# Optimization experiments

Hardware: AMD Instinct MI355X
Metric: run time of the kernel (lower is better)

The kernel has to match this reference:

```python
import jax, jax.numpy as jnp
import numpy as np

M, N, DIM, B = 32000, 2048, 1024, 2048  # vocab, hidden, embed dim, batch
SIGMA = 20.0


def setup_inputs() -> dict:
    key = jax.random.key(0)
    ks = jax.random.split(key, 16)
    u = lambda k, shape: jax.random.uniform(k, shape, dtype=jnp.float32)
    return {
        "input_text": jax.random.randint(ks[0], (B,), 0, M),
        "h_prev": jax.random.normal(ks[1], (N, B), dtype=jnp.float32),
        "C_prev": jax.random.normal(ks[2], (N, B), dtype=jnp.float32),
        "emb": jax.random.normal(ks[3], (M, DIM), dtype=jnp.float32),
        "W_A": u(ks[4], (M, N)) / SIGMA,
        "W_C": u(ks[5], (N, N + DIM)) / SIGMA,
        "W_f": u(ks[6], (N, N + DIM)) / SIGMA,
        "W_o": u(ks[7], (N, N + DIM)) / SIGMA,
        "W_i": u(ks[8], (N, N + DIM)) / SIGMA,
        "b_A": u(ks[9], (M, 1)),
        "b_C": u(ks[10], (N, 1)),
        "b_f": u(ks[11], (N, 1)),
        "b_o": u(ks[12], (N, 1)),
        "b_i": u(ks[13], (N, 1)),
    }


def reference(input_text, h_prev, C_prev, emb, W_A, W_C, W_f, W_o, W_i,
              b_A, b_C, b_f, b_o, b_i):
    x = emb[input_text].T                     # [dim, B]
    z = jnp.concatenate([h_prev, x], axis=0)  # [n+dim, B]
    f = jax.nn.sigmoid(W_f @ z + b_f)
    i = jax.nn.sigmoid(W_i @ z + b_i)
    o = jax.nn.sigmoid(W_o @ z + b_o)
    tildeC = jnp.tanh(W_C @ z + b_C)
    C = f * C_prev + i * tildeC
    h = o * jnp.tanh(C)
    y = W_A @ h + b_A                         # [m, B]
    return (y, h, C)
```

## Files before the change

### kernel.cpp

```cpp
#include <hip/hip_runtime.h>

#define DM 32000
#define DN 2048
#define DD 1024
#define DB 2048
#define DKG 3072

typedef __attribute__((ext_vector_type(4))) float floatx4;
typedef __attribute__((ext_vector_type(8))) short shortx8;

__device__ inline unsigned int f2bf(float f) {
    unsigned int u = __builtin_bit_cast(unsigned int, f);
    u += 0x7fffu + ((u >> 16) & 1u);
    return u >> 16;
}

__device__ inline unsigned int cvt_pk_bf16(float lo, float hi) {
    unsigned int r;
    asm("v_cvt_pk_bf16_f32 %0, %1, %2" : "=v"(r) : "v"(lo), "v"(hi));
    return r;
}

__device__ inline void gld_lds16(const void* g, void* l) {
    __builtin_amdgcn_global_load_lds(
        (const __attribute__((address_space(1))) unsigned int*)g,
        (__attribute__((address_space(3))) unsigned int*)l,
        16, 0, 0);
}

__device__ inline float fast_sigmoid(float x) { return 1.0f / (1.0f + __expf(-x)); }
__device__ inline float fast_tanh(float x) { return 1.0f - 2.0f / (__expf(2.0f * x) + 1.0f); }

__global__ __launch_bounds__(256) void transpose_h_kernel(
    const float* __restrict__ h_prev, unsigned short* __restrict__ z_t)
{
    __shared__ unsigned short T[64 * 66];
    int t = threadIdx.x;
    int b0 = blockIdx.x * 64, k0 = blockIdx.y * 64;
    int bi = t & 63, wv = t >> 6;
    #pragma unroll
    for (int i = 0; i < 16; i++) {
        int kl = wv + i * 4;
        float v = h_prev[(size_t)(k0 + kl) * DB + b0 + bi];
        T[kl * 66 + bi] = (unsigned short)f2bf(v);
    }
    __syncthreads();
    #pragma unroll
    for (int i = 0; i < 16; i++) {
        int r = wv + i * 4;
        z_t[(size_t)(b0 + r) * DKG + k0 + bi] = T[bi * 66 + r];
    }
}

__global__ __launch_bounds__(256) void emb_gather_kernel(
    const int* __restrict__ idx, const float* __restrict__ emb,
    unsigned short* __restrict__ z_t)
{
    int b = blockIdx.x;
    int row = idx[b];
    int t = threadIdx.x;
    const floatx4 v = *(const floatx4*)(&emb[(size_t)row * DD + t * 4]);
    unsigned int p0 = (f2bf(v[1]) << 16) | f2bf(v[0]);
    unsigned int p1 = (f2bf(v[3]) << 16) | f2bf(v[2]);
    *(uint2*)(&z_t[(size_t)b * DKG + DN + t * 4]) = make_uint2(p0, p1);
}

__global__ __launch_bounds__(256) void wconv_kernel(
    const float* __restrict__ src, unsigned short* __restrict__ dst)
{
    size_t i = ((size_t)blockIdx.x * 256 + threadIdx.x) * 8;
    floatx4 v0 = *(const floatx4*)(src + i);
    floatx4 v1 = *(const floatx4*)(src + i + 4);
    uint4 p;
    p.x = cvt_pk_bf16(v0[0], v0[1]);
    p.y = cvt_pk_bf16(v0[2], v0[3]);
    p.z = cvt_pk_bf16(v1[0], v1[1]);
    p.w = cvt_pk_bf16(v1[2], v1[3]);
    *(uint4*)(dst + i) = p;
}


__global__ __launch_bounds__(256, 3) void gemm_wa_kernel(
    const unsigned short* __restrict__ A, const unsigned short* __restrict__ Bt,
    float* __restrict__ C, const float* __restrict__ bias)
{
    __shared__ unsigned short As[128 * 64];
    __shared__ unsigned short Bs[128 * 64];
    const int K = DN;
    int t = threadIdx.x;
    int lane = t & 63, wave = t >> 6;
    int wm = (wave >> 1) * 64, wn = (wave & 1) * 64;
    size_t m0 = (size_t)blockIdx.y * 128, n0 = (size_t)blockIdx.x * 128;
    int mrow = lane & 15, kgrp = lane >> 4, l7 = lane & 7;
    int r8 = t >> 3, lsl = t & 7;
    int ss = lsl ^ (r8 & 7);

    floatx4 acc[4][4] = {};

    for (int k0 = 0; k0 < K; k0 += 64) {
        #pragma unroll
        for (int i = 0; i < 4; i++) {
            int row = i * 32 + r8;
            gld_lds16(A  + (m0 + row) * (size_t)K + k0 + ss * 8,
                      &As[(i * 256 + wave * 64) * 8]);
            gld_lds16(Bt + (n0 + row) * (size_t)K + k0 + ss * 8,
                      &Bs[(i * 256 + wave * 64) * 8]);
        }
        __syncthreads();
        #pragma unroll
        for (int ks = 0; ks < 2; ks++) {
            int so = ((ks * 4 + kgrp) ^ l7) * 8;
            shortx8 af[4], bfv[4];
            #pragma unroll
            for (int mi = 0; mi < 4; mi++)
                af[mi] = *(const shortx8*)(&As[(wm + mi * 16 + mrow) * 64 + so]);
            #pragma unroll
            for (int ni = 0; ni < 4; ni++)
                bfv[ni] = *(const shortx8*)(&Bs[(wn + ni * 16 + mrow) * 64 + so]);
            #pragma unroll
            for (int mi = 0; mi < 4; mi++)
                #pragma unroll
                for (int ni = 0; ni < 4; ni++)
                    acc[mi][ni] = __builtin_amdgcn_mfma_f32_16x16x32_bf16(
                        af[mi], bfv[ni], acc[mi][ni], 0, 0, 0);
        }
        __syncthreads();
    }

    int cn = lane & 15, rb = kgrp * 4;
    #pragma unroll
    for (int mi = 0; mi < 4; mi++) {
        #pragma unroll
        for (int r = 0; r < 4; r++) {
            size_t row = m0 + wm + mi * 16 + rb + r;
            float bv = bias[row];
            #pragma unroll
            for (int ni = 0; ni < 4; ni++)
                C[row * DB + n0 + wn + ni * 16 + cn] = acc[mi][ni][r] + bv;
        }
    }
}

__global__ __launch_bounds__(256, 3) void gemm_gates_kernel(
    const float* __restrict__ A0, const float* __restrict__ A1,
    const float* __restrict__ A2, const float* __restrict__ A3,
    const unsigned short* __restrict__ Bt,
    float* __restrict__ C0, float* __restrict__ C1,
    float* __restrict__ C2, float* __restrict__ C3)
{
    __shared__ unsigned short As[128 * 64];
    __shared__ unsigned short Bs[128 * 64];
    const int K = DKG;
    int t = threadIdx.x;
    int lane = t & 63, wave = t >> 6;
    int wm = (wave >> 1) * 64, wn = (wave & 1) * 64;
    int zz = blockIdx.z;
    const float* A = (zz == 0) ? A0 : (zz == 1) ? A1 : (zz == 2) ? A2 : A3;
    float* Cout    = (zz == 0) ? C0 : (zz == 1) ? C1 : (zz == 2) ? C2 : C3;
    size_t m0 = (size_t)blockIdx.y * 128, n0 = (size_t)blockIdx.x * 128;
    int mrow = lane & 15, kgrp = lane >> 4, l7 = lane & 7;
    int r8 = t >> 3, lsl = t & 7;
    int ss = lsl ^ (r8 & 7);

    floatx4 acc[4][4] = {};

    for (int k0 = 0; k0 < K; k0 += 64) {
        #pragma unroll
        for (int i = 0; i < 4; i++) {
            int row = i * 32 + r8;
            gld_lds16(Bt + (n0 + row) * (size_t)K + k0 + ss * 8,
                      &Bs[(i * 256 + wave * 64) * 8]);
        }
        #pragma unroll
        for (int i = 0; i < 4; i++) {
            int row = i * 32 + r8;
            const float* src = A + (m0 + row) * (size_t)K + k0 + lsl * 8;
            floatx4 v0 = *(const floatx4*)(src);
            floatx4 v1 = *(const floatx4*)(src + 4);
            uint4 p;
            p.x = cvt_pk_bf16(v0[0], v0[1]);
            p.y = cvt_pk_bf16(v0[2], v0[3]);
            p.z = cvt_pk_bf16(v1[0], v1[1]);
            p.w = cvt_pk_bf16(v1[2], v1[3]);
            *(uint4*)(&As[(row * 8 + ss) * 8]) = p;
        }
        __syncthreads();
        #pragma unroll
        for (int ks = 0; ks < 2; ks++) {
            int so = ((ks * 4 + kgrp) ^ l7) * 8;
            shortx8 af[4], bfv[4];
            #pragma unroll
            for (int mi = 0; mi < 4; mi++)
                af[mi] = *(const shortx8*)(&As[(wm + mi * 16 + mrow) * 64 + so]);
            #pragma unroll
            for (int ni = 0; ni < 4; ni++)
                bfv[ni] = *(const shortx8*)(&Bs[(wn + ni * 16 + mrow) * 64 + so]);
            #pragma unroll
            for (int mi = 0; mi < 4; mi++)
                #pragma unroll
                for (int ni = 0; ni < 4; ni++)
                    acc[mi][ni] = __builtin_amdgcn_mfma_f32_16x16x32_bf16(
                        af[mi], bfv[ni], acc[mi][ni], 0, 0, 0);
        }
        __syncthreads();
    }

    int cn = lane & 15, rb = kgrp * 4;
    #pragma unroll
    for (int mi = 0; mi < 4; mi++) {
        #pragma unroll
        for (int r = 0; r < 4; r++) {
            size_t row = m0 + wm + mi * 16 + rb + r;
            #pragma unroll
            for (int ni = 0; ni < 4; ni++)
                Cout[row * DB + n0 + wn + ni * 16 + cn] = acc[mi][ni][r];
        }
    }
}

__global__ __launch_bounds__(256) void pointwise_kernel(
    const float* __restrict__ Pf, const float* __restrict__ Pi,
    const float* __restrict__ Po, const float* __restrict__ Pc,
    const float* __restrict__ C_prev,
    const float* __restrict__ b_f, const float* __restrict__ b_i,
    const float* __restrict__ b_o, const float* __restrict__ b_C,
    float* __restrict__ outH, float* __restrict__ outC,
    unsigned short* __restrict__ h_t)
{
    __shared__ unsigned short T[64 * 66];
    int t = threadIdx.x;
    int b0 = blockIdx.x * 64, n0 = blockIdx.y * 64;
    int bi = t & 63, wv = t >> 6;
    #pragma unroll
    for (int i = 0; i < 16; i++) {
        int nl = wv + i * 4;
        size_t idx = (size_t)(n0 + nl) * DB + b0 + bi;
        float f  = fast_sigmoid(Pf[idx] + b_f[n0 + nl]);
        float ii = fast_sigmoid(Pi[idx] + b_i[n0 + nl]);
        float o  = fast_sigmoid(Po[idx] + b_o[n0 + nl]);
        float tc = fast_tanh(Pc[idx] + b_C[n0 + nl]);
        float C  = f * C_prev[idx] + ii * tc;
        float h  = o * fast_tanh(C);
        outC[idx] = C;
        outH[idx] = h;
        T[nl * 66 + bi] = (unsigned short)f2bf(h);
    }
    __syncthreads();
    #pragma unroll
    for (int i = 0; i < 16; i++) {
        int r = wv + i * 4;
        h_t[(size_t)(b0 + r) * DN + n0 + bi] = T[bi * 66 + r];
    }
}

extern "C" void kernel_launch(void* const* d_in, const int* in_sizes, int n_in,
                              void* d_out, int out_size, void* d_ws, size_t ws_size,
                              hipStream_t stream)
{
    const int*   input_text = (const int*)d_in[0];
    const float* h_prev = (const float*)d_in[1];
    const float* C_prev = (const float*)d_in[2];
    const float* emb    = (const float*)d_in[3];
    const float* W_A    = (const float*)d_in[4];
    const float* W_C    = (const float*)d_in[5];
    const float* W_f    = (const float*)d_in[6];
    const float* W_o    = (const float*)d_in[7];
    const float* W_i    = (const float*)d_in[8];
    const float* b_A    = (const float*)d_in[9];
    const float* b_C    = (const float*)d_in[10];
    const float* b_f    = (const float*)d_in[11];
    const float* b_o    = (const float*)d_in[12];
    const float* b_i    = (const float*)d_in[13];

    char* ws = (char*)d_ws;
    unsigned short* z_t = (unsigned short*)ws;
    float* Pf = (float*)(ws + 12582912);
    float* Pi = (float*)(ws + 12582912 + 1 * 16777216);
    float* Po = (float*)(ws + 12582912 + 2 * 16777216);
    float* Pc = (float*)(ws + 12582912 + 3 * 16777216);
    unsigned short* h_t = (unsigned short*)(ws + 12582912 + 4 * 16777216);
    unsigned short* wa  = (unsigned short*)ws;

    float* y    = (float*)d_out;
    float* outH = y + (size_t)DM * DB;
    float* outC = outH + (size_t)DN * DB;

    transpose_h_kernel<<<dim3(32, 32), 256, 0, stream>>>(h_prev, z_t);
    emb_gather_kernel<<<dim3(2048), 256, 0, stream>>>(input_text, emb, z_t);

    gemm_gates_kernel<<<dim3(16, 16, 4), 256, 0, stream>>>(
        W_f, W_i, W_o, W_C, z_t, Pf, Pi, Po, Pc);

    pointwise_kernel<<<dim3(32, 32), 256, 0, stream>>>(
        Pf, Pi, Po, Pc, C_prev, b_f, b_i, b_o, b_C, outH, outC, h_t);

    wconv_kernel<<<dim3(16000), 256, 0, stream>>>(W_A, wa);
    gemm_wa_kernel<<<dim3(16, 125), 256, 0, stream>>>(wa, h_t, y, b_A);
    wconv_kernel<<<dim3(16000), 256, 0, stream>>>(W_A + (size_t)16000 * DN, wa);
    gemm_wa_kernel<<<dim3(16, 125), 256, 0, stream>>>(
        wa, h_t, y + (size_t)16000 * DB, b_A + 16000);
}
```

Before: 1.023 ms.

## Pre-convert gate weights to bf16 and unify GEMMs with XCD-aware tile swizzle

The four gate weight matrices are converted to bf16 up front, into the output y buffer used as scratch, and stacked. The gate GEMM then becomes one launch of a shared bf16 GEMM kernel that loads A asynchronously straight into LDS, instead of converting fp32 A in registers inside the K loop. The shared kernel also remaps block IDs so that blocks scheduled on the same XCD work on contiguous tiles, aiming for better L2 reuse, and it handles an optional bias. The cost is extra conversion passes over about 100 MB of fp32 weights plus the writes of their bf16 copies.

Measured after the change: 979.3 us. 1.04x faster.

```diff
diff --git a/kernel.cpp b/kernel.cpp
--- a/kernel.cpp
+++ b/kernel.cpp
@@ -79,18 +79,21 @@
     *(uint4*)(dst + i) = p;
 }
 
-
-__global__ __launch_bounds__(256, 3) void gemm_wa_kernel(
+__global__ __launch_bounds__(256, 3) void gemm_bt16_kernel(
     const unsigned short* __restrict__ A, const unsigned short* __restrict__ Bt,
-    float* __restrict__ C, const float* __restrict__ bias)
+    float* __restrict__ C, const float* __restrict__ bias, int K)
 {
     __shared__ unsigned short As[128 * 64];
     __shared__ unsigned short Bs[128 * 64];
-    const int K = DN;
     int t = threadIdx.x;
     int lane = t & 63, wave = t >> 6;
     int wm = (wave >> 1) * 64, wn = (wave & 1) * 64;
-    size_t m0 = (size_t)blockIdx.y * 128, n0 = (size_t)blockIdx.x * 128;
+
+    int nwg = gridDim.x * gridDim.y;
+    int flat = blockIdx.y * gridDim.x + blockIdx.x;
+    int swz = (flat & 7) * (nwg >> 3) + (flat >> 3);
+    size_t m0 = (size_t)(swz >> 4) * 128, n0 = (size_t)(swz & 15) * 128;
+
     int mrow = lane & 15, kgrp = lane >> 4, l7 = lane & 7;
     int r8 = t >> 3, lsl = t & 7;
     int ss = lsl ^ (r8 & 7);
@@ -133,87 +136,10 @@
         #pragma unroll
         for (int r = 0; r < 4; r++) {
             size_t row = m0 + wm + mi * 16 + rb + r;
-            float bv = bias[row];
+            float bv = bias ? bias[row] : 0.0f;
             #pragma unroll
             for (int ni = 0; ni < 4; ni++)
                 C[row * DB + n0 + wn + ni * 16 + cn] = acc[mi][ni][r] + bv;
-        }
-    }
-}
-
-__global__ __launch_bounds__(256, 3) void gemm_gates_kernel(
-    const float* __restrict__ A0, const float* __restrict__ A1,
-    const float* __restrict__ A2, const float* __restrict__ A3,
-    const unsigned short* __restrict__ Bt,
-    float* __restrict__ C0, float* __restrict__ C1,
-    float* __restrict__ C2, float* __restrict__ C3)
-{
-    __shared__ unsigned short As[128 * 64];
-    __shared__ unsigned short Bs[128 * 64];
-    const int K = DKG;
-    int t = threadIdx.x;
-    int lane = t & 63, wave = t >> 6;
-    int wm = (wave >> 1) * 64, wn = (wave & 1) * 64;
-    int zz = blockIdx.z;
-    const float* A = (zz == 0) ? A0 : (zz == 1) ? A1 : (zz == 2) ? A2 : A3;
-    float* Cout    = (zz == 0) ? C0 : (zz == 1) ? C1 : (zz == 2) ? C2 : C3;
-    size_t m0 = (size_t)blockIdx.y * 128, n0 = (size_t)blockIdx.x * 128;
-    int mrow = lane & 15, kgrp = lane >> 4, l7 = lane & 7;
-    int r8 = t >> 3, lsl = t & 7;
-    int ss = lsl ^ (r8 & 7);
-
-    floatx4 acc[4][4] = {};
-
-    for (int k0 = 0; k0 < K; k0 += 64) {
-        #pragma unroll
-        for (int i = 0; i < 4; i++) {
-            int row = i * 32 + r8;
-            gld_lds16(Bt + (n0 + row) * (size_t)K + k0 + ss * 8,
-                      &Bs[(i * 256 + wave * 64) * 8]);
-        }
-        #pragma unroll
-        for (int i = 0; i < 4; i++) {
-            int row = i * 32 + r8;
-            const float* src = A + (m0 + row) * (size_t)K + k0 + lsl * 8;
-            floatx4 v0 = *(const floatx4*)(src);
-            floatx4 v1 = *(const floatx4*)(src + 4);
-            uint4 p;
-            p.x = cvt_pk_bf16(v0[0], v0[1]);
-            p.y = cvt_pk_bf16(v0[2], v0[3]);
-            p.z = cvt_pk_bf16(v1[0], v1[1]);
-            p.w = cvt_pk_bf16(v1[2], v1[3]);
-            *(uint4*)(&As[(row * 8 + ss) * 8]) = p;
-        }
-        __syncthreads();
-        #pragma unroll
-        for (int ks = 0; ks < 2; ks++) {
-            int so = ((ks * 4 + kgrp) ^ l7) * 8;
-            shortx8 af[4], bfv[4];
-            #pragma unroll
-            for (int mi = 0; mi < 4; mi++)
-                af[mi] = *(const shortx8*)(&As[(wm + mi * 16 + mrow) * 64 + so]);
-            #pragma unroll
-            for (int ni = 0; ni < 4; ni++)
-                bfv[ni] = *(const shortx8*)(&Bs[(wn + ni * 16 + mrow) * 64 + so]);
-            #pragma unroll
-            for (int mi = 0; mi < 4; mi++)
-                #pragma unroll
-                for (int ni = 0; ni < 4; ni++)
-                    acc[mi][ni] = __builtin_amdgcn_mfma_f32_16x16x32_bf16(
-                        af[mi], bfv[ni], acc[mi][ni], 0, 0, 0);
-        }
-        __syncthreads();
-    }
-
-    int cn = lane & 15, rb = kgrp * 4;
-    #pragma unroll
-    for (int mi = 0; mi < 4; mi++) {
-        #pragma unroll
-        for (int r = 0; r < 4; r++) {
-            size_t row = m0 + wm + mi * 16 + rb + r;
-            #pragma unroll
-            for (int ni = 0; ni < 4; ni++)
-                Cout[row * DB + n0 + wn + ni * 16 + cn] = acc[mi][ni][r];
         }
     }
 }
@@ -274,7 +200,8 @@
 
     char* ws = (char*)d_ws;
     unsigned short* z_t = (unsigned short*)ws;
-    float* Pf = (float*)(ws + 12582912);
+    float* P  = (float*)(ws + 12582912);
+    float* Pf = P;
     float* Pi = (float*)(ws + 12582912 + 1 * 16777216);
     float* Po = (float*)(ws + 12582912 + 2 * 16777216);
     float* Pc = (float*)(ws + 12582912 + 3 * 16777216);
@@ -285,18 +212,26 @@
     float* outH = y + (size_t)DM * DB;
     float* outC = outH + (size_t)DN * DB;
 
+    unsigned short* wg = (unsigned short*)y;
+
+    const size_t WGN = (size_t)DN * DKG;
+    wconv_kernel<<<dim3(3072), 256, 0, stream>>>(W_f, wg + 0 * WGN);
+    wconv_kernel<<<dim3(3072), 256, 0, stream>>>(W_i, wg + 1 * WGN);
+    wconv_kernel<<<dim3(3072), 256, 0, stream>>>(W_o, wg + 2 * WGN);
+    wconv_kernel<<<dim3(3072), 256, 0, stream>>>(W_C, wg + 3 * WGN);
+
     transpose_h_kernel<<<dim3(32, 32), 256, 0, stream>>>(h_prev, z_t);
     emb_gather_kernel<<<dim3(2048), 256, 0, stream>>>(input_text, emb, z_t);
 
-    gemm_gates_kernel<<<dim3(16, 16, 4), 256, 0, stream>>>(
-        W_f, W_i, W_o, W_C, z_t, Pf, Pi, Po, Pc);
+    gemm_bt16_kernel<<<dim3(16, 64), 256, 0, stream>>>(
+        wg, z_t, P, nullptr, DKG);
 
     pointwise_kernel<<<dim3(32, 32), 256, 0, stream>>>(
         Pf, Pi, Po, Pc, C_prev, b_f, b_i, b_o, b_C, outH, outC, h_t);
 
     wconv_kernel<<<dim3(16000), 256, 0, stream>>>(W_A, wa);
-    gemm_wa_kernel<<<dim3(16, 125), 256, 0, stream>>>(wa, h_t, y, b_A);
+    gemm_bt16_kernel<<<dim3(16, 125), 256, 0, stream>>>(wa, h_t, y, b_A, DN);
     wconv_kernel<<<dim3(16000), 256, 0, stream>>>(W_A + (size_t)16000 * DN, wa);
-    gemm_wa_kernel<<<dim3(16, 125), 256, 0, stream>>>(
-        wa, h_t, y + (size_t)16000 * DB, b_A + 16000);
-}
+    gemm_bt16_kernel<<<dim3(16, 125), 256, 0, stream>>>(
+        wa, h_t, y + (size_t)16000 * DB, b_A + 16000, DN);
+}
```
